# Optimization experiments

Measured on AMD Instinct MI355X. Metric: run time of the kernel, lower is better.

## Reference

```python
import jax, jax.numpy as jnp
import numpy as np

B, T, C = 4, 2048, 1024
N_HEAD = 16
HEAD_DIM = C // N_HEAD
SCALE = 1.0 / np.sqrt(HEAD_DIM).astype(np.float32)


def setup_inputs() -> dict:
    key = jax.random.key(0)
    k1, k2, k3 = jax.random.split(key, 3)
    x = jax.random.normal(k1, (B, T, C), dtype=jnp.float32)
    # torch Linear weights: [out_features, in_features], scaled init
    w_qkv = jax.random.normal(k2, (3 * C, C), dtype=jnp.float32) * (1.0 / np.sqrt(C))
    w_out = jax.random.normal(k3, (C, C), dtype=jnp.float32) * (1.0 / np.sqrt(C))
    b_out = jnp.zeros((C,), dtype=jnp.float32)
    return {"x": x, "w_qkv": w_qkv, "w_out": w_out, "b_out": b_out}


def reference(x, w_qkv, w_out, b_out):
    Bsz, Tlen, Cdim = x.shape
    qkv = jnp.einsum('btc,oc->bto', x, w_qkv)  # [B,T,3C]
    q, k, v = jnp.split(qkv, 3, axis=-1)
    # [B,H,T,D]
    def heads(t):
        return t.reshape(Bsz, Tlen, N_HEAD, HEAD_DIM).transpose(0, 2, 1, 3)
    q, k, v = heads(q), heads(k), heads(v)
    att = jnp.einsum('bhqd,bhkd->bhqk', q, k) * SCALE  # [B,H,T,T]
    causal = jnp.tril(jnp.ones((Tlen, Tlen), dtype=bool))
    att = jnp.where(causal[None, None], att, -jnp.inf)
    att = jax.nn.softmax(att, axis=-1)
    out = jnp.einsum('bhqk,bhkd->bhqd', att, v)
    out = out.transpose(0, 2, 1, 3).reshape(Bsz, Tlen, Cdim)
    out = jnp.einsum('btc,oc->bto', out, w_out) + b_out
    return out
```

## Files before the change

kernel.cpp:

```cpp
#include <hip/hip_runtime.h>
#include <stdint.h>


typedef __attribute__((ext_vector_type(8))) short bf16x8;
typedef __attribute__((ext_vector_type(4))) float f32x4;

#define EXP2F(x) __builtin_amdgcn_exp2f(x)
#define SL2E 0.18033688011112042f
#define FIXED_M 15.0f

__device__ __forceinline__ short f2bf(float f) {
  union { float f; unsigned u; } c; c.f = f;
  unsigned u = c.u;
  unsigned r = (u + 0x7fffu + ((u >> 16) & 1u)) >> 16;
  return (short)(unsigned short)r;
}

__device__ __forceinline__ short f2bf_trunc(float f) {
  union { float f; unsigned u; } c; c.f = f;
  return (short)(unsigned short)(c.u >> 16);
}

__device__ __forceinline__ void llds16(const short* g, short* l) {
  __builtin_amdgcn_global_load_lds(
      (const __attribute__((address_space(1))) unsigned int*)g,
      (__attribute__((address_space(3))) unsigned int*)l, 16, 0, 0);
}

__global__ __launch_bounds__(256) void cast_f32_to_bf16(
    const float* __restrict__ src, short* __restrict__ dst, int n4) {
  int i = blockIdx.x * 256 + threadIdx.x;
  if (i >= n4) return;
  float4 f = ((const float4*)src)[i];
  short4 o;
  o.x = f2bf(f.x); o.y = f2bf(f.y); o.z = f2bf(f.z); o.w = f2bf(f.w);
  ((short4*)dst)[i] = o;
}

__global__ __launch_bounds__(256) void gemm_qkv(
    const short* __restrict__ A, const short* __restrict__ Bw,
    short* __restrict__ Qo, short* __restrict__ Ko, short* __restrict__ Vt) {
  const int K = 1024;
  __shared__ short smem[17408];
  const int tid = threadIdx.x;
  const int lane = tid & 63;
  const int wave = tid >> 6;
  const int m0 = blockIdx.y * 128;
  const int n0 = blockIdx.x * 128;
  const int wm = (wave >> 1) * 64;
  const int wn = (wave & 1) * 64;
  const int mrow = lane & 15;
  const int kq = lane >> 4;

  f32x4 acc[4][4];
#pragma unroll
  for (int i = 0; i < 4; ++i)
#pragma unroll
    for (int j = 0; j < 4; ++j) acc[i][j] = (f32x4){0.f, 0.f, 0.f, 0.f};

  auto stage = [&](int it, int buf) {
#pragma unroll
    for (int call = 0; call < 2; ++call) {
      const int cb = call * 256 + wave * 64;
      const int c = cb + lane;
      const int row = c >> 2;
      const int scol = (c & 3) ^ (row & 3);
      llds16(A + (size_t)(m0 + row) * K + it * 32 + scol * 8,
             &smem[buf * 8192 + cb * 8]);
      llds16(Bw + (size_t)(n0 + row) * K + it * 32 + scol * 8,
             &smem[buf * 8192 + 4096 + cb * 8]);
    }
  };

  stage(0, 0);
  __syncthreads();

  for (int it = 0; it < 32; ++it) {
    const int buf = it & 1;
    if (it < 31) stage(it + 1, buf ^ 1);
    const short* lA = &smem[buf * 8192];
    const short* lB = &smem[buf * 8192 + 4096];
    bf16x8 af[4], bfr[4];
#pragma unroll
    for (int i = 0; i < 4; ++i) {
      const int row = wm + i * 16 + mrow;
      af[i] = *(const bf16x8*)&lA[row * 32 + ((kq ^ (row & 3)) * 8)];
    }
#pragma unroll
    for (int j = 0; j < 4; ++j) {
      const int row = wn + j * 16 + mrow;
      bfr[j] = *(const bf16x8*)&lB[row * 32 + ((kq ^ (row & 3)) * 8)];
    }
#pragma unroll
    for (int i = 0; i < 4; ++i)
#pragma unroll
      for (int j = 0; j < 4; ++j)
        acc[i][j] = __builtin_amdgcn_mfma_f32_16x16x32_bf16(af[i], bfr[j], acc[i][j], 0, 0, 0);
    __syncthreads();
  }

  const int b = m0 >> 11;
  if (n0 < 2048) {
    short* lC = smem;
#pragma unroll
    for (int i = 0; i < 4; ++i) {
      const int row = wm + i * 16 + kq * 4;
#pragma unroll
      for (int j = 0; j < 4; ++j) {
        const int col = wn + j * 16 + mrow;
        const float sc_ = (((n0 + col) >> 10) == 1) ? SL2E : 1.0f;
#pragma unroll
        for (int r = 0; r < 4; ++r)
          lC[(row + r) * 132 + col] = f2bf(acc[i][j][r] * sc_);
      }
    }
    __syncthreads();
#pragma unroll
    for (int call = 0; call < 8; ++call) {
      const int cc = call * 256 + tid;
      const int row = cc >> 4;
      const int t = (m0 + row) & 2047;
      const int o = n0 + (cc & 15) * 8;
      const int c = o & 1023;
      const int h = c >> 6;
      const int d = c & 63;
      short* dst = (o >> 10) == 0 ? Qo : Ko;
      bf16x8 val = *(const bf16x8*)&lC[row * 132 + (cc & 15) * 8];
      *(bf16x8*)(dst + ((size_t)(b * 16 + h) * 2048 + t) * 64 + d) = val;
    }
  } else {
    short* lCt = smem;
#pragma unroll
    for (int i = 0; i < 4; ++i) {
      const int row = wm + i * 16 + kq * 4;
#pragma unroll
      for (int j = 0; j < 4; ++j) {
        const int col = wn + j * 16 + mrow;
#pragma unroll
        for (int r = 0; r < 4; ++r)
          lCt[col * 136 + row + r] = f2bf(acc[i][j][r]);
      }
    }
    __syncthreads();
#pragma unroll
    for (int call = 0; call < 8; ++call) {
      const int cc = call * 256 + tid;
      const int col = cc >> 4;
      const int tg = cc & 15;
      const int o = n0 + col;
      const int d = o & 63;
      const int h = (o >> 6) & 15;
      const int t = (m0 & 2047) + tg * 8;
      bf16x8 val = *(const bf16x8*)&lCt[col * 136 + tg * 8];
      *(bf16x8*)(Vt + ((size_t)(b * 16 + h) * 64 + d) * 2048 + t) = val;
    }
  }
}

__global__ __launch_bounds__(256) void gemm_out(
    const short* __restrict__ A, const short* __restrict__ Bw,
    const float* __restrict__ bias, float* __restrict__ Out) {
  const int K = 1024;
  __shared__ short smem[16384];
  const int tid = threadIdx.x;
  const int lane = tid & 63;
  const int wave = tid >> 6;
  const int m0 = blockIdx.y * 128;
  const int n0 = blockIdx.x * 128;
  const int wm = (wave >> 1) * 64;
  const int wn = (wave & 1) * 64;
  const int mrow = lane & 15;
  const int kq = lane >> 4;

  f32x4 acc[4][4];
#pragma unroll
  for (int i = 0; i < 4; ++i)
#pragma unroll
    for (int j = 0; j < 4; ++j) acc[i][j] = (f32x4){0.f, 0.f, 0.f, 0.f};

  auto stage = [&](int it, int buf) {
#pragma unroll
    for (int call = 0; call < 2; ++call) {
      const int cb = call * 256 + wave * 64;
      const int c = cb + lane;
      const int row = c >> 2;
      const int scol = (c & 3) ^ (row & 3);
      llds16(A + (size_t)(m0 + row) * K + it * 32 + scol * 8,
             &smem[buf * 8192 + cb * 8]);
      llds16(Bw + (size_t)(n0 + row) * K + it * 32 + scol * 8,
             &smem[buf * 8192 + 4096 + cb * 8]);
    }
  };

  stage(0, 0);
  __syncthreads();

  for (int it = 0; it < 32; ++it) {
    const int buf = it & 1;
    if (it < 31) stage(it + 1, buf ^ 1);
    const short* lA = &smem[buf * 8192];
    const short* lB = &smem[buf * 8192 + 4096];
    bf16x8 af[4], bfr[4];
#pragma unroll
    for (int i = 0; i < 4; ++i) {
      const int row = wm + i * 16 + mrow;
      af[i] = *(const bf16x8*)&lA[row * 32 + ((kq ^ (row & 3)) * 8)];
    }
#pragma unroll
    for (int j = 0; j < 4; ++j) {
      const int row = wn + j * 16 + mrow;
      bfr[j] = *(const bf16x8*)&lB[row * 32 + ((kq ^ (row & 3)) * 8)];
    }
#pragma unroll
    for (int i = 0; i < 4; ++i)
#pragma unroll
      for (int j = 0; j < 4; ++j)
        acc[i][j] = __builtin_amdgcn_mfma_f32_16x16x32_bf16(af[i], bfr[j], acc[i][j], 0, 0, 0);
    __syncthreads();
  }

#pragma unroll
  for (int i = 0; i < 4; ++i) {
    const int m = m0 + wm + i * 16 + kq * 4;
#pragma unroll
    for (int j = 0; j < 4; ++j) {
      const int n = n0 + wn + j * 16 + mrow;
      const float bb = bias[n];
#pragma unroll
      for (int r = 0; r < 4; ++r)
        Out[(size_t)(m + r) * 1024 + n] = acc[i][j][r] + bb;
    }
  }
}

__global__ __launch_bounds__(256) void flash_attn(
    const short* __restrict__ Qg, const short* __restrict__ Kg,
    const short* __restrict__ Vtg, short* __restrict__ Og) {
  const int T = 2048;
  __shared__ short lK[2][64 * 64];
  __shared__ short lVt[2][64 * 64];
  __shared__ short lP[4 * 16 * 76];
  const int tid = threadIdx.x;
  const int lane = tid & 63;
  const int wave = tid >> 6;
  const int bh = blockIdx.x;
  const int bx = blockIdx.y;
  const int mrow = lane & 15;
  const int kq = lane >> 4;
  const int swz = mrow & 7;
  const size_t base = (size_t)bh * T * 64;
  const size_t vbase = (size_t)bh * 64 * T;

  int qts[4];
  qts[0] = bx;
  qts[1] = 31 - bx;
  qts[2] = 15 - bx;
  qts[3] = 16 + bx;

  const bf16x8 ones = {0x3F80, 0x3F80, 0x3F80, 0x3F80, 0x3F80, 0x3F80, 0x3F80, 0x3F80};

  bf16x8 aq0[4], aq1[4];
#pragma unroll
  for (int s = 0; s < 4; ++s) {
    const short* qp = Qg + base + (size_t)(qts[s] * 64 + wave * 16 + mrow) * 64 + kq * 8;
    aq0[s] = *(const bf16x8*)qp;
    aq1[s] = *(const bf16x8*)(qp + 32);
  }

  f32x4 acc[4][4], lac[4];
#pragma unroll
  for (int s = 0; s < 4; ++s) {
    lac[s] = (f32x4){0.f, 0.f, 0.f, 0.f};
#pragma unroll
    for (int jd = 0; jd < 4; ++jd) acc[s][jd] = (f32x4){0.f, 0.f, 0.f, 0.f};
  }

  auto stage = [&](int nt, int buf) {
#pragma unroll
    for (int call = 0; call < 2; ++call) {
      const int cb = call * 256 + wave * 64;
      const int c = cb + lane;
      const int row = c >> 3;
      const int scol = (c & 7) ^ (row & 7);
      llds16(Kg + base + (size_t)(nt * 64 + row) * 64 + scol * 8, &lK[buf][cb * 8]);
      llds16(Vtg + vbase + (size_t)row * T + nt * 64 + scol * 8, &lVt[buf][cb * 8]);
    }
  };

  stage(0, 0);
  __syncthreads();

  const int ktmax = qts[1];
  for (int kt = 0; kt <= ktmax; ++kt) {
    const int bcur = kt & 1;
    if (kt < ktmax) stage(kt + 1, bcur ^ 1);
    const short* K_ = lK[bcur];
    const short* Vt_ = lVt[bcur];

#pragma unroll
    for (int s = 0; s < 4; ++s) {
      const int qt = qts[s];
      if (kt > qt) continue;

      f32x4 sc[4];
#pragma unroll
      for (int j = 0; j < 4; ++j) {
        const short* krow = &K_[(j * 16 + mrow) * 64];
        bf16x8 kb0 = *(const bf16x8*)&krow[(kq ^ swz) * 8];
        bf16x8 kb1 = *(const bf16x8*)&krow[((4 + kq) ^ swz) * 8];
        f32x4 ss = (f32x4){-FIXED_M, -FIXED_M, -FIXED_M, -FIXED_M};
        ss = __builtin_amdgcn_mfma_f32_16x16x32_bf16(aq0[s], kb0, ss, 0, 0, 0);
        ss = __builtin_amdgcn_mfma_f32_16x16x32_bf16(aq1[s], kb1, ss, 0, 0, 0);
        sc[j] = ss;
      }

      if (kt == qt) {
        const int qrow = qt * 64 + wave * 16 + kq * 4;
#pragma unroll
        for (int j = 0; j < 4; ++j) {
          const int key = kt * 64 + j * 16 + mrow;
#pragma unroll
          for (int r = 0; r < 4; ++r)
            if (key > qrow + r) sc[j][r] = -1e30f;
        }
      }

      short* pw = &lP[wave * 1216];
#pragma unroll
      for (int j = 0; j < 4; ++j)
#pragma unroll
        for (int r = 0; r < 4; ++r)
          pw[(kq * 4 + r) * 76 + j * 16 + mrow] = f2bf_trunc(EXP2F(sc[j][r]));

      bf16x8 pa0 = *(const bf16x8*)&lP[wave * 1216 + mrow * 76 + kq * 8];
      bf16x8 pa1 = *(const bf16x8*)&lP[wave * 1216 + mrow * 76 + 32 + kq * 8];
      lac[s] = __builtin_amdgcn_mfma_f32_16x16x32_bf16(pa0, ones, lac[s], 0, 0, 0);
      lac[s] = __builtin_amdgcn_mfma_f32_16x16x32_bf16(pa1, ones, lac[s], 0, 0, 0);
#pragma unroll
      for (int jd = 0; jd < 4; ++jd) {
        const short* vrow = &Vt_[(jd * 16 + mrow) * 64];
        bf16x8 vb0 = *(const bf16x8*)&vrow[(kq ^ swz) * 8];
        bf16x8 vb1 = *(const bf16x8*)&vrow[((4 + kq) ^ swz) * 8];
        acc[s][jd] = __builtin_amdgcn_mfma_f32_16x16x32_bf16(pa0, vb0, acc[s][jd], 0, 0, 0);
        acc[s][jd] = __builtin_amdgcn_mfma_f32_16x16x32_bf16(pa1, vb1, acc[s][jd], 0, 0, 0);
      }
    }
    __syncthreads();
  }

  const int b = bh >> 4;
  const int h = bh & 15;
#pragma unroll
  for (int s = 0; s < 4; ++s) {
#pragma unroll
    for (int r = 0; r < 4; ++r) {
      const float inv = 1.0f / lac[s][r];
      const int t = qts[s] * 64 + wave * 16 + kq * 4 + r;
#pragma unroll
      for (int jd = 0; jd < 4; ++jd) {
        const int col = h * 64 + jd * 16 + mrow;
        Og[((size_t)b * 2048 + t) * 1024 + col] = f2bf(acc[s][jd][r] * inv);
      }
    }
  }
}

extern "C" void kernel_launch(void* const* d_in, const int* in_sizes, int n_in,
                              void* d_out, int out_size, void* d_ws, size_t ws_size,
                              hipStream_t stream) {
  const float* x = (const float*)d_in[0];
  const float* w_qkv = (const float*)d_in[1];
  const float* w_out = (const float*)d_in[2];
  const float* b_out = (const float*)d_in[3];
  float* out = (float*)d_out;

  char* ws = (char*)d_ws;
  const size_t NX = 8192ull * 1024;
  const size_t NWQ = 3072ull * 1024;
  const size_t NWO = 1024ull * 1024;
  const size_t NQ = 64ull * 2048 * 64;
  size_t off = 0;
  short* xb    = (short*)(ws + off); off += NX * 2;
  short* wqkvb = (short*)(ws + off); off += NWQ * 2;
  short* woutb = (short*)(ws + off); off += NWO * 2;
  short* q     = (short*)(ws + off); off += NQ * 2;
  short* k     = (short*)(ws + off); off += NQ * 2;
  short* vt    = (short*)(ws + off); off += NQ * 2;
  short* attb  = (short*)(ws + off); off += NX * 2;
  if (off > ws_size) return;

  cast_f32_to_bf16<<<(int)(NX / 4 / 256), 256, 0, stream>>>(x, xb, (int)(NX / 4));
  cast_f32_to_bf16<<<(int)(NWQ / 4 / 256), 256, 0, stream>>>(w_qkv, wqkvb, (int)(NWQ / 4));
  cast_f32_to_bf16<<<(int)(NWO / 4 / 256), 256, 0, stream>>>(w_out, woutb, (int)(NWO / 4));
  gemm_qkv<<<dim3(24, 64), 256, 0, stream>>>(xb, wqkvb, q, k, vt);
  flash_attn<<<dim3(64, 8), 256, 0, stream>>>(q, k, vt, attb);
  gemm_out<<<dim3(8, 64), 256, 0, stream>>>(attb, woutb, b_out, out);
}
```

Baseline: 266.1 us.

## Keep softmax probabilities in registers via transposed QK^T and permuted K rows

The score MFMA now computes S^T, with K as the A operand, and K rows are loaded into LDS in a permuted order. This puts each lane's exp results directly in the layout needed for the PV MFMA A operand, so the LDS round-trip for P is gone. Probabilities are packed with v_cvt_pk_bf16_f32, which rounds instead of truncating. Each block now handles two query tiles instead of four, and the grid doubles to raise parallelism. s_setprio is placed around MFMA groups to favour matrix issue.

Result: faster. 255.1 us (-4.1%).

```diff
diff --git a/kernel.cpp b/kernel.cpp
--- a/kernel.cpp
+++ b/kernel.cpp
@@ -8,6 +8,8 @@
 #define EXP2F(x) __builtin_amdgcn_exp2f(x)
 #define SL2E 0.18033688011112042f
 #define FIXED_M 15.0f
+
+template <bool B> struct BoolC { static constexpr bool value = B; };
 
 __device__ __forceinline__ short f2bf(float f) {
   union { float f; unsigned u; } c; c.f = f;
@@ -16,9 +18,23 @@
   return (short)(unsigned short)r;
 }
 
-__device__ __forceinline__ short f2bf_trunc(float f) {
-  union { float f; unsigned u; } c; c.f = f;
-  return (short)(unsigned short)(c.u >> 16);
+__device__ __forceinline__ void softmax_pack(const f32x4* sc, bf16x8& pa0, bf16x8& pa1) {
+  union U { int i[4]; bf16x8 v; };
+  U u0, u1;
+#pragma unroll
+  for (int j = 0; j < 4; ++j) {
+    float p0 = EXP2F(sc[j][0]);
+    float p1 = EXP2F(sc[j][1]);
+    float p2 = EXP2F(sc[j][2]);
+    float p3 = EXP2F(sc[j][3]);
+    int w0, w1;
+    asm("v_cvt_pk_bf16_f32 %0, %1, %2" : "=v"(w0) : "v"(p0), "v"(p1));
+    asm("v_cvt_pk_bf16_f32 %0, %1, %2" : "=v"(w1) : "v"(p2), "v"(p3));
+    if (j < 2) { u0.i[j * 2] = w0; u0.i[j * 2 + 1] = w1; }
+    else       { u1.i[(j - 2) * 2] = w0; u1.i[(j - 2) * 2 + 1] = w1; }
+  }
+  pa0 = u0.v;
+  pa1 = u1.v;
 }
 
 __device__ __forceinline__ void llds16(const short* g, short* l) {
@@ -239,7 +255,6 @@
   const int T = 2048;
   __shared__ short lK[2][64 * 64];
   __shared__ short lVt[2][64 * 64];
-  __shared__ short lP[4 * 16 * 76];
   const int tid = threadIdx.x;
   const int lane = tid & 63;
   const int wave = tid >> 6;
@@ -251,28 +266,28 @@
   const size_t base = (size_t)bh * T * 64;
   const size_t vbase = (size_t)bh * 64 * T;
 
-  int qts[4];
-  qts[0] = bx;
-  qts[1] = 31 - bx;
-  qts[2] = 15 - bx;
-  qts[3] = 16 + bx;
+  const int qt0 = bx;
+  const int qt1 = 31 - bx;
 
   const bf16x8 ones = {0x3F80, 0x3F80, 0x3F80, 0x3F80, 0x3F80, 0x3F80, 0x3F80, 0x3F80};
 
-  bf16x8 aq0[4], aq1[4];
-#pragma unroll
-  for (int s = 0; s < 4; ++s) {
-    const short* qp = Qg + base + (size_t)(qts[s] * 64 + wave * 16 + mrow) * 64 + kq * 8;
-    aq0[s] = *(const bf16x8*)qp;
-    aq1[s] = *(const bf16x8*)(qp + 32);
-  }
-
-  f32x4 acc[4][4], lac[4];
-#pragma unroll
-  for (int s = 0; s < 4; ++s) {
-    lac[s] = (f32x4){0.f, 0.f, 0.f, 0.f};
-#pragma unroll
-    for (int jd = 0; jd < 4; ++jd) acc[s][jd] = (f32x4){0.f, 0.f, 0.f, 0.f};
+  bf16x8 aq0_0, aq1_0, aq0_1, aq1_1;
+  {
+    const short* qp0 = Qg + base + (size_t)(qt0 * 64 + wave * 16 + mrow) * 64 + kq * 8;
+    aq0_0 = *(const bf16x8*)qp0;
+    aq1_0 = *(const bf16x8*)(qp0 + 32);
+    const short* qp1 = Qg + base + (size_t)(qt1 * 64 + wave * 16 + mrow) * 64 + kq * 8;
+    aq0_1 = *(const bf16x8*)qp1;
+    aq1_1 = *(const bf16x8*)(qp1 + 32);
+  }
+
+  f32x4 acc0[4], acc1[4], lac0, lac1;
+  lac0 = (f32x4){0.f, 0.f, 0.f, 0.f};
+  lac1 = (f32x4){0.f, 0.f, 0.f, 0.f};
+#pragma unroll
+  for (int jd = 0; jd < 4; ++jd) {
+    acc0[jd] = (f32x4){0.f, 0.f, 0.f, 0.f};
+    acc1[jd] = (f32x4){0.f, 0.f, 0.f, 0.f};
   }
 
   auto stage = [&](int nt, int buf) {
@@ -282,7 +297,8 @@
       const int c = cb + lane;
       const int row = c >> 3;
       const int scol = (c & 7) ^ (row & 7);
-      llds16(Kg + base + (size_t)(nt * 64 + row) * 64 + scol * 8, &lK[buf][cb * 8]);
+      const int grow = (row & 0x23) | ((row & 0x0C) << 1) | ((row & 0x10) >> 2);
+      llds16(Kg + base + (size_t)(nt * 64 + grow) * 64 + scol * 8, &lK[buf][cb * 8]);
       llds16(Vtg + vbase + (size_t)row * T + nt * 64 + scol * 8, &lVt[buf][cb * 8]);
     }
   };
@@ -290,77 +306,102 @@
   stage(0, 0);
   __syncthreads();
 
-  const int ktmax = qts[1];
-  for (int kt = 0; kt <= ktmax; ++kt) {
+  auto seg = [&](auto A, const short* K_, const short* Vt_, int kt) {
+    constexpr bool ACT0 = decltype(A)::value;
+    f32x4 sc0[4], sc1[4];
+#pragma unroll
+    for (int j = 0; j < 4; ++j) {
+      const short* krow = &K_[(j * 16 + mrow) * 64];
+      bf16x8 kb0 = *(const bf16x8*)&krow[(kq ^ swz) * 8];
+      bf16x8 kb1 = *(const bf16x8*)&krow[((4 + kq) ^ swz) * 8];
+      __builtin_amdgcn_s_setprio(1);
+      f32x4 ss = (f32x4){-FIXED_M, -FIXED_M, -FIXED_M, -FIXED_M};
+      ss = __builtin_amdgcn_mfma_f32_16x16x32_bf16(kb0, aq0_1, ss, 0, 0, 0);
+      ss = __builtin_amdgcn_mfma_f32_16x16x32_bf16(kb1, aq1_1, ss, 0, 0, 0);
+      sc1[j] = ss;
+      if constexpr (ACT0) {
+        f32x4 s2 = (f32x4){-FIXED_M, -FIXED_M, -FIXED_M, -FIXED_M};
+        s2 = __builtin_amdgcn_mfma_f32_16x16x32_bf16(kb0, aq0_0, s2, 0, 0, 0);
+        s2 = __builtin_amdgcn_mfma_f32_16x16x32_bf16(kb1, aq1_0, s2, 0, 0, 0);
+        sc0[j] = s2;
+      }
+      __builtin_amdgcn_s_setprio(0);
+    }
+
+    if (kt == qt1) {
+      const int qcol = qt1 * 64 + wave * 16 + mrow;
+#pragma unroll
+      for (int j = 0; j < 4; ++j) {
+        const int keyb = kt * 64 + ((j & 2) << 4) + (kq << 3) + ((j & 1) << 2);
+#pragma unroll
+        for (int r = 0; r < 4; ++r)
+          if (keyb + r > qcol) sc1[j][r] = -1e30f;
+      }
+    }
+    if constexpr (ACT0) {
+      if (kt == qt0) {
+        const int qcol = qt0 * 64 + wave * 16 + mrow;
+#pragma unroll
+        for (int j = 0; j < 4; ++j) {
+          const int keyb = kt * 64 + ((j & 2) << 4) + (kq << 3) + ((j & 1) << 2);
+#pragma unroll
+          for (int r = 0; r < 4; ++r)
+            if (keyb + r > qcol) sc0[j][r] = -1e30f;
+        }
+      }
+    }
+
+    bf16x8 pa0_1, pa1_1, pa0_0, pa1_0;
+    softmax_pack(sc1, pa0_1, pa1_1);
+    lac1 = __builtin_amdgcn_mfma_f32_16x16x32_bf16(pa0_1, ones, lac1, 0, 0, 0);
+    lac1 = __builtin_amdgcn_mfma_f32_16x16x32_bf16(pa1_1, ones, lac1, 0, 0, 0);
+    if constexpr (ACT0) {
+      softmax_pack(sc0, pa0_0, pa1_0);
+      lac0 = __builtin_amdgcn_mfma_f32_16x16x32_bf16(pa0_0, ones, lac0, 0, 0, 0);
+      lac0 = __builtin_amdgcn_mfma_f32_16x16x32_bf16(pa1_0, ones, lac0, 0, 0, 0);
+    }
+
+#pragma unroll
+    for (int jd = 0; jd < 4; ++jd) {
+      const short* vrow = &Vt_[(jd * 16 + mrow) * 64];
+      bf16x8 vb0 = *(const bf16x8*)&vrow[(kq ^ swz) * 8];
+      bf16x8 vb1 = *(const bf16x8*)&vrow[((4 + kq) ^ swz) * 8];
+      __builtin_amdgcn_s_setprio(1);
+      acc1[jd] = __builtin_amdgcn_mfma_f32_16x16x32_bf16(pa0_1, vb0, acc1[jd], 0, 0, 0);
+      acc1[jd] = __builtin_amdgcn_mfma_f32_16x16x32_bf16(pa1_1, vb1, acc1[jd], 0, 0, 0);
+      if constexpr (ACT0) {
+        acc0[jd] = __builtin_amdgcn_mfma_f32_16x16x32_bf16(pa0_0, vb0, acc0[jd], 0, 0, 0);
+        acc0[jd] = __builtin_amdgcn_mfma_f32_16x16x32_bf16(pa1_0, vb1, acc0[jd], 0, 0, 0);
+      }
+      __builtin_amdgcn_s_setprio(0);
+    }
+  };
+
+  for (int kt = 0; kt <= qt1; ++kt) {
     const int bcur = kt & 1;
-    if (kt < ktmax) stage(kt + 1, bcur ^ 1);
-    const short* K_ = lK[bcur];
-    const short* Vt_ = lVt[bcur];
-
-#pragma unroll
-    for (int s = 0; s < 4; ++s) {
-      const int qt = qts[s];
-      if (kt > qt) continue;
-
-      f32x4 sc[4];
-#pragma unroll
-      for (int j = 0; j < 4; ++j) {
-        const short* krow = &K_[(j * 16 + mrow) * 64];
-        bf16x8 kb0 = *(const bf16x8*)&krow[(kq ^ swz) * 8];
-        bf16x8 kb1 = *(const bf16x8*)&krow[((4 + kq) ^ swz) * 8];
-        f32x4 ss = (f32x4){-FIXED_M, -FIXED_M, -FIXED_M, -FIXED_M};
-        ss = __builtin_amdgcn_mfma_f32_16x16x32_bf16(aq0[s], kb0, ss, 0, 0, 0);
-        ss = __builtin_amdgcn_mfma_f32_16x16x32_bf16(aq1[s], kb1, ss, 0, 0, 0);
-        sc[j] = ss;
-      }
-
-      if (kt == qt) {
-        const int qrow = qt * 64 + wave * 16 + kq * 4;
-#pragma unroll
-        for (int j = 0; j < 4; ++j) {
-          const int key = kt * 64 + j * 16 + mrow;
-#pragma unroll
-          for (int r = 0; r < 4; ++r)
-            if (key > qrow + r) sc[j][r] = -1e30f;
-        }
-      }
-
-      short* pw = &lP[wave * 1216];
-#pragma unroll
-      for (int j = 0; j < 4; ++j)
-#pragma unroll
-        for (int r = 0; r < 4; ++r)
-          pw[(kq * 4 + r) * 76 + j * 16 + mrow] = f2bf_trunc(EXP2F(sc[j][r]));
-
-      bf16x8 pa0 = *(const bf16x8*)&lP[wave * 1216 + mrow * 76 + kq * 8];
-      bf16x8 pa1 = *(const bf16x8*)&lP[wave * 1216 + mrow * 76 + 32 + kq * 8];
-      lac[s] = __builtin_amdgcn_mfma_f32_16x16x32_bf16(pa0, ones, lac[s], 0, 0, 0);
-      lac[s] = __builtin_amdgcn_mfma_f32_16x16x32_bf16(pa1, ones, lac[s], 0, 0, 0);
-#pragma unroll
-      for (int jd = 0; jd < 4; ++jd) {
-        const short* vrow = &Vt_[(jd * 16 + mrow) * 64];
-        bf16x8 vb0 = *(const bf16x8*)&vrow[(kq ^ swz) * 8];
-        bf16x8 vb1 = *(const bf16x8*)&vrow[((4 + kq) ^ swz) * 8];
-        acc[s][jd] = __builtin_amdgcn_mfma_f32_16x16x32_bf16(pa0, vb0, acc[s][jd], 0, 0, 0);
-        acc[s][jd] = __builtin_amdgcn_mfma_f32_16x16x32_bf16(pa1, vb1, acc[s][jd], 0, 0, 0);
-      }
-    }
+    if (kt < qt1) stage(kt + 1, bcur ^ 1);
+    if (kt <= qt0) seg(BoolC<true>{}, lK[bcur], lVt[bcur], kt);
+    else           seg(BoolC<false>{}, lK[bcur], lVt[bcur], kt);
     __syncthreads();
   }
 
   const int b = bh >> 4;
   const int h = bh & 15;
 #pragma unroll
-  for (int s = 0; s < 4; ++s) {
-#pragma unroll
-    for (int r = 0; r < 4; ++r) {
-      const float inv = 1.0f / lac[s][r];
-      const int t = qts[s] * 64 + wave * 16 + kq * 4 + r;
-#pragma unroll
-      for (int jd = 0; jd < 4; ++jd) {
-        const int col = h * 64 + jd * 16 + mrow;
-        Og[((size_t)b * 2048 + t) * 1024 + col] = f2bf(acc[s][jd][r] * inv);
-      }
+  for (int r = 0; r < 4; ++r) {
+    const float inv0 = 1.0f / lac0[r];
+    const int t0 = qt0 * 64 + wave * 16 + kq * 4 + r;
+#pragma unroll
+    for (int jd = 0; jd < 4; ++jd) {
+      const int col = h * 64 + jd * 16 + mrow;
+      Og[((size_t)b * 2048 + t0) * 1024 + col] = f2bf(acc0[jd][r] * inv0);
+    }
+    const float inv1 = 1.0f / lac1[r];
+    const int t1 = qt1 * 64 + wave * 16 + kq * 4 + r;
+#pragma unroll
+    for (int jd = 0; jd < 4; ++jd) {
+      const int col = h * 64 + jd * 16 + mrow;
+      Og[((size_t)b * 2048 + t1) * 1024 + col] = f2bf(acc1[jd][r] * inv1);
     }
   }
 }
@@ -393,6 +434,6 @@
   cast_f32_to_bf16<<<(int)(NWQ / 4 / 256), 256, 0, stream>>>(w_qkv, wqkvb, (int)(NWQ / 4));
   cast_f32_to_bf16<<<(int)(NWO / 4 / 256), 256, 0, stream>>>(w_out, woutb, (int)(NWO / 4));
   gemm_qkv<<<dim3(24, 64), 256, 0, stream>>>(xb, wqkvb, q, k, vt);
-  flash_attn<<<dim3(64, 8), 256, 0, stream>>>(q, k, vt, attb);
+  flash_attn<<<dim3(64, 16), 256, 0, stream>>>(q, k, vt, attb);
   gemm_out<<<dim3(8, 64), 256, 0, stream>>>(attb, woutb, b_out, out);
 }
```
